# Optimization experiments

Hardware: AMD Instinct MI355X
Metric: run time of the kernel (lower is better)

The kernel has to match this reference:

```python
import jax, jax.numpy as jnp
import numpy as np

B, S, E, H = 1, 4096, 768, 12
D = E // H  # head_dim = 64


def setup_inputs() -> dict:
    key = jax.random.key(0)
    ks = jax.random.split(key, 6)
    scale = 0.02
    x = jax.random.normal(ks[0], (B, S, E), dtype=jnp.float32)
    Wq = jax.random.normal(ks[1], (E, E), dtype=jnp.float32) * scale
    Wk = jax.random.normal(ks[2], (E, E), dtype=jnp.float32) * scale
    Wv = jax.random.normal(ks[3], (E, E), dtype=jnp.float32) * scale
    Wo = jax.random.normal(ks[4], (E, E), dtype=jnp.float32) * scale
    bo = jax.random.normal(ks[5], (E,), dtype=jnp.float32) * scale
    mask = jnp.tril(jnp.ones((S, S), dtype=bool))[None, None]  # [1,1,S,S] causal
    return {"x": x, "Wq": Wq, "Wk": Wk, "Wv": Wv, "Wo": Wo, "bo": bo, "mask": mask}


def reference(x, Wq, Wk, Wv, Wo, bo, mask):
    # projections (torch Linear: y = x @ W.T; here W stored as [E,E] applied as x@W)
    q = jnp.einsum('bse,ef->bsf', x, Wq).reshape(B, S, H, D).transpose(0, 2, 1, 3)
    k = jnp.einsum('bse,ef->bsf', x, Wk).reshape(B, S, H, D).transpose(0, 2, 1, 3)
    v = jnp.einsum('bse,ef->bsf', x, Wv).reshape(B, S, H, D).transpose(0, 2, 1, 3)
    scores = jnp.einsum('bhqd,bhkd->bhqk', q, k) / jnp.sqrt(jnp.float32(D))
    scores = jnp.where(mask, scores, -jnp.inf)
    attn = jax.nn.softmax(scores, axis=-1)  # dropout p=0 -> identity
    ctx = jnp.einsum('bhqk,bhkd->bhqd', attn, v)
    ctx = ctx.transpose(0, 2, 1, 3).reshape(B, S, E)
    return jnp.einsum('bse,ef->bsf', ctx, Wo) + bo
```

## Files before the change

### kernel.cpp

```cpp
#include <hip/hip_runtime.h>
#include <math.h>

#define S 4096
#define E 768
#define H 12
#define Dh 64
#define SCALE2 0.1803368801111204f

typedef short short8 __attribute__((ext_vector_type(8)));
typedef float floatx4 __attribute__((ext_vector_type(4)));

__device__ __forceinline__ unsigned short f2bf(float f) {
    union { float f; unsigned int i; } c; c.f = f;
    unsigned int i = c.i;
    return (unsigned short)((i + 0x7fffu + ((i >> 16) & 1u)) >> 16);
}

__device__ __forceinline__ unsigned int pk_bf16(float lo, float hi) {
#if __has_builtin(__builtin_amdgcn_cvt_pk_bf16_f32)
    typedef __bf16 bf16x2 __attribute__((ext_vector_type(2)));
    union { bf16x2 v; unsigned int u; } c;
    c.v = __builtin_amdgcn_cvt_pk_bf16_f32(lo, hi);
    return c.u;
#else
    union { float f; unsigned int i; } a, b; a.f = lo; b.f = hi;
    return ((a.i + 0x8000u) >> 16) | ((b.i + 0x8000u) & 0xFFFF0000u);
#endif
}

__device__ __forceinline__ unsigned int scale_pk(unsigned int u, float s) {
    union { unsigned int i; float f; } lo, hi;
    lo.i = u << 16; hi.i = u & 0xffff0000u;
    return pk_bf16(lo.f * s, hi.f * s);
}

__device__ __forceinline__ void pk_atomic_add_bf16(unsigned short* addr, unsigned int bits) {
    unsigned long long a = (unsigned long long)addr;
    asm volatile("global_atomic_pk_add_bf16 %0, %1, off" :: "v"(a), "v"(bits) : "memory");
}

__device__ __forceinline__ void gload_lds16(const unsigned short* g, unsigned short* l) {
    __builtin_amdgcn_global_load_lds(
        (const __attribute__((address_space(1))) unsigned int*)g,
        (__attribute__((address_space(3))) unsigned int*)l, 16, 0, 0);
}

__device__ __forceinline__ void pl32swap(unsigned &a, unsigned &b) {
#if __has_builtin(__builtin_amdgcn_permlane32_swap)
    typedef unsigned uint2v __attribute__((ext_vector_type(2)));
    uint2v r = __builtin_amdgcn_permlane32_swap(a, b, false, false);
    a = r[0]; b = r[1];
#else
    asm("s_nop 1\n\tv_permlane32_swap_b32 %0, %1\n\ts_nop 1" : "+v"(a), "+v"(b));
#endif
}
__device__ __forceinline__ void pl16swap(unsigned &a, unsigned &b) {
#if __has_builtin(__builtin_amdgcn_permlane16_swap)
    typedef unsigned uint2v __attribute__((ext_vector_type(2)));
    uint2v r = __builtin_amdgcn_permlane16_swap(a, b, false, false);
    a = r[0]; b = r[1];
#else
    asm("s_nop 1\n\tv_permlane16_swap_b32 %0, %1\n\ts_nop 1" : "+v"(a), "+v"(b));
#endif
}

__device__ __forceinline__ short8 quad_redist(unsigned a0, unsigned a1, unsigned a2, unsigned a3) {
    pl32swap(a0, a2); pl16swap(a0, a2);
    pl32swap(a1, a3); pl16swap(a1, a3);
    union { unsigned u[4]; short8 s; } r;
    r.u[0] = a0; r.u[1] = a1; r.u[2] = a2; r.u[3] = a3;
    return r.s;
}

__global__ __launch_bounds__(256)
void prep_kernel(const float* __restrict__ x, unsigned short* __restrict__ xb,
                 const float* __restrict__ s0, const float* __restrict__ s1,
                 const float* __restrict__ s2, const float* __restrict__ s3,
                 unsigned short* __restrict__ d0, unsigned short* __restrict__ d1,
                 unsigned short* __restrict__ d2, unsigned short* __restrict__ d3,
                 char* __restrict__ zbase) {
    __shared__ unsigned short tile[32][33];
    const int b = blockIdx.x;
    const int tid = threadIdx.x;
    if (b < 2304) {
        int z = b / 576, rem = b - z * 576;
        int bx = rem % 24, by = rem / 24;
        const float* src = (z == 0) ? s0 : (z == 1) ? s1 : (z == 2) ? s2 : s3;
        unsigned short* dst = (z == 0) ? d0 : (z == 1) ? d1 : (z == 2) ? d2 : d3;
        int tx = tid & 31, ty = tid >> 5;
        int xcol = bx * 32 + tx;
        int y0 = by * 32;
        for (int j = ty; j < 32; j += 8)
            tile[j][tx] = f2bf(src[(size_t)(y0 + j) * E + xcol]);
        __syncthreads();
        int x2 = y0 + tx;
        int y2 = bx * 32;
        for (int j = ty; j < 32; j += 8)
            dst[(size_t)(y2 + j) * E + x2] = tile[tx][j];
    } else if (b < 3840) {
        int i = ((b - 2304) * 256 + tid) * 8;
        float4 f0 = *reinterpret_cast<const float4*>(x + i);
        float4 f1 = *reinterpret_cast<const float4*>(x + i + 4);
        unsigned short u[8];
        u[0]=f2bf(f0.x); u[1]=f2bf(f0.y); u[2]=f2bf(f0.z); u[3]=f2bf(f0.w);
        u[4]=f2bf(f1.x); u[5]=f2bf(f1.y); u[6]=f2bf(f1.z); u[7]=f2bf(f1.w);
        *reinterpret_cast<uint4*>(xb + i) = *reinterpret_cast<uint4*>(u);
    } else {
        size_t i = (size_t)(b - 3840) * 16384 + (size_t)tid * 64;
        uint4 z4 = make_uint4(0u, 0u, 0u, 0u);
        *reinterpret_cast<uint4*>(zbase + i)      = z4;
        *reinterpret_cast<uint4*>(zbase + i + 16) = z4;
        *reinterpret_cast<uint4*>(zbase + i + 32) = z4;
        *reinterpret_cast<uint4*>(zbase + i + 48) = z4;
    }
}

__global__ __launch_bounds__(256)
void gemm_qkv(const unsigned short* __restrict__ A,
              const unsigned short* __restrict__ BT,
              unsigned short* __restrict__ Qb, unsigned short* __restrict__ Kb,
              unsigned short* __restrict__ VTb) {
    __shared__ unsigned short Asm[2][128 * 64];
    __shared__ unsigned short Bsm[128 * 64];
    const int tid  = threadIdx.x;
    const int wave = tid >> 6, lane = tid & 63;
    const int quad = lane >> 4, l16 = lane & 15;
    const int lrow = lane >> 3, lchunk = lane & 7;
    const int bb = blockIdx.x;
    const int xcd = bb & 7, j = bb >> 3;
    const int mt = (xcd >> 1) * 8 + (j & 7);
    const int nt = (xcd & 1) * 9 + (j >> 3);
    const int n0 = nt * 128;
    const int m0 = mt * 128;
    const int aw = wave >> 1, bw = wave & 1;

    floatx4 acc[4][4];
    #pragma unroll
    for (int at = 0; at < 4; at++)
        #pragma unroll
        for (int ct = 0; ct < 4; ct++)
            #pragma unroll
            for (int r = 0; r < 4; r++) acc[at][ct][r] = 0.f;

    auto stageA = [&](int k0, int buf) {
        #pragma unroll
        for (int i = 0; i < 4; i++) {
            int rbase = wave * 32 + i * 8;
            int row   = rbase + lrow;
            int gc    = lchunk ^ (row & 7);
            gload_lds16(&A[(size_t)(m0 + row) * E + k0 + gc * 8], &Asm[buf][rbase * 64]);
        }
    };
    auto stageB = [&](int k0) {
        #pragma unroll
        for (int i = 0; i < 4; i++) {
            int rbase = wave * 32 + i * 8;
            int row   = rbase + lrow;
            int gc    = lchunk ^ (row & 7);
            gload_lds16(&BT[(size_t)(n0 + row) * E + k0 + gc * 8], &Bsm[rbase * 64]);
        }
    };

    stageA(0, 0);
    __builtin_amdgcn_sched_barrier(0);
    stageB(0);
    __builtin_amdgcn_sched_barrier(0);
    stageA(64, 1);
    __builtin_amdgcn_sched_barrier(0);

    for (int ki = 0; ki < 12; ki++) {
        const int cur = ki & 1;
        if (ki < 11) { asm volatile("s_waitcnt vmcnt(4)" ::: "memory"); }
        else         { asm volatile("s_waitcnt vmcnt(0)" ::: "memory"); }
        asm volatile("s_waitcnt lgkmcnt(0)" ::: "memory");
        __builtin_amdgcn_sched_barrier(0);
        __builtin_amdgcn_s_barrier();
        __builtin_amdgcn_sched_barrier(0);

        const unsigned short* As = Asm[cur];
        #pragma unroll
        for (int kk = 0; kk < 2; kk++) {
            const int g = kk * 4 + quad;
            short8 af[4], bfr[4];
            #pragma unroll
            for (int t = 0; t < 4; t++) {
                int ar = aw * 64 + t * 16 + l16;
                af[t]  = *reinterpret_cast<const short8*>(&As[ar * 64 + (g ^ (ar & 7)) * 8]);
                int br = bw * 64 + t * 16 + l16;
                bfr[t] = *reinterpret_cast<const short8*>(&Bsm[br * 64 + (g ^ (br & 7)) * 8]);
            }
            #pragma unroll
            for (int at = 0; at < 4; at++)
                #pragma unroll
                for (int ct = 0; ct < 4; ct++)
                    acc[at][ct] = __builtin_amdgcn_mfma_f32_16x16x32_bf16(af[at], bfr[ct], acc[at][ct], 0, 0, 0);
        }

        if (ki < 11) {
            __builtin_amdgcn_s_barrier();
            __builtin_amdgcn_sched_barrier(0);
            stageB((ki + 1) * 64);
            __builtin_amdgcn_sched_barrier(0);
            if (ki < 10) stageA((ki + 2) * 64, cur);
            __builtin_amdgcn_sched_barrier(0);
        }
    }

    const int sec = n0 / 768;
    const int nb  = n0 - sec * 768 + bw * 64;
    if (sec == 2) {
        #pragma unroll
        for (int at = 0; at < 4; at++)
            #pragma unroll
            for (int ct = 0; ct < 4; ct++) {
                int nsec = nb + ct * 16 + l16, hh = nsec >> 6, d = nsec & 63;
                int s0i = m0 + aw * 64 + at * 16 + quad * 4;
                uint2 w2;
                w2.x = pk_bf16(acc[at][ct][0], acc[at][ct][1]);
                w2.y = pk_bf16(acc[at][ct][2], acc[at][ct][3]);
                *reinterpret_cast<uint2*>(&VTb[(size_t)hh * Dh * S + (size_t)d * S + s0i]) = w2;
            }
    } else {
        #pragma unroll
        for (int at = 0; at < 4; at++)
            #pragma unroll
            for (int ct = 0; ct < 4; ct++) {
                int nsec = nb + ct * 16 + l16, hh = nsec >> 6, d = nsec & 63;
                #pragma unroll
                for (int r = 0; r < 4; r++) {
                    int s = m0 + aw * 64 + at * 16 + quad * 4 + r;
                    float v = acc[at][ct][r];
                    if (sec == 0) Qb[(size_t)hh * S * Dh + (size_t)s * Dh + d] = f2bf(v * SCALE2);
                    else          Kb[(size_t)hh * S * Dh + (size_t)s * Dh + d] = f2bf(v);
                }
            }
    }
}

__global__ __launch_bounds__(256)
void gemm_out(const unsigned short* __restrict__ ctxp,
              const unsigned short* __restrict__ BT,
              const float* __restrict__ lsumf,
              float* __restrict__ outp, const float* __restrict__ bias) {
    __shared__ unsigned short Asm[2][128 * 64];
    __shared__ unsigned short Bsm[2][64 * 64];
    const int tid  = threadIdx.x;
    const int wave = tid >> 6, lane = tid & 63;
    const int quad = lane >> 4, l16 = lane & 15;
    const int lrow = lane >> 3, lchunk = lane & 7;
    const int bb = blockIdx.x;
    const int xcd = bb & 7, j = bb >> 3;
    const int mt = (xcd >> 1) * 8 + (j & 7);
    const int nt = (xcd & 1) * 6 + (j >> 3);
    const int n0 = nt * 64;
    const int m0 = mt * 128;
    const int arow = tid >> 1, ahalf = tid & 1;

    floatx4 acc[2][4];
    #pragma unroll
    for (int at = 0; at < 2; at++)
        #pragma unroll
        for (int ct = 0; ct < 4; ct++)
            #pragma unroll
            for (int r = 0; r < 4; r++) acc[at][ct][r] = 0.f;

    uint4 au[4]; float lf;
    auto loadA = [&](int k0) {
        const unsigned short* asrc = ctxp + (size_t)(m0 + arow) * E + k0 + ahalf * 32;
        au[0] = *reinterpret_cast<const uint4*>(asrc + 0);
        au[1] = *reinterpret_cast<const uint4*>(asrc + 8);
        au[2] = *reinterpret_cast<const uint4*>(asrc + 16);
        au[3] = *reinterpret_cast<const uint4*>(asrc + 24);
        lf = lsumf[(k0 >> 6) * S + m0 + arow];
    };
    auto writeA = [&](int buf) {
        float linv = 1.0f / lf;
        #pragma unroll
        for (int cc = 0; cc < 4; cc++) {
            uint4 w;
            w.x = scale_pk(au[cc].x, linv);
            w.y = scale_pk(au[cc].y, linv);
            w.z = scale_pk(au[cc].z, linv);
            w.w = scale_pk(au[cc].w, linv);
            int chunk = ahalf * 4 + cc;
            *reinterpret_cast<uint4*>(&Asm[buf][arow * 64 + (chunk ^ (arow & 7)) * 8]) = w;
        }
    };
    auto stageB = [&](int k0, int buf) {
        #pragma unroll
        for (int i = 0; i < 2; i++) {
            int rbase = wave * 16 + i * 8;
            int row   = rbase + lrow;
            int gc    = lchunk ^ (row & 7);
            gload_lds16(&BT[(size_t)(n0 + row) * E + k0 + gc * 8], &Bsm[buf][rbase * 64]);
        }
    };

    loadA(0);
    __builtin_amdgcn_sched_barrier(0);
    asm volatile("s_waitcnt vmcnt(0)" ::: "memory");
    writeA(0);
    __builtin_amdgcn_sched_barrier(0);
    stageB(0, 0);
    __builtin_amdgcn_sched_barrier(0);
    loadA(64);
    __builtin_amdgcn_sched_barrier(0);

    for (int ki = 0; ki < 12; ki++) {
        const int cur = ki & 1, nxt = cur ^ 1;
        if (ki <= 10) { asm volatile("s_waitcnt vmcnt(5)" ::: "memory"); }
        else          { asm volatile("s_waitcnt vmcnt(0)" ::: "memory"); }
        asm volatile("s_waitcnt lgkmcnt(0)" ::: "memory");
        __builtin_amdgcn_sched_barrier(0);
        __builtin_amdgcn_s_barrier();
        __builtin_amdgcn_sched_barrier(0);
        asm volatile("s_waitcnt vmcnt(0)" ::: "memory");
        if (ki < 11) writeA(nxt);
        __builtin_amdgcn_sched_barrier(0);
        if (ki < 11) stageB((ki + 1) * 64, nxt);
        if (ki <= 9) loadA((ki + 2) * 64);
        __builtin_amdgcn_sched_barrier(0);

        const unsigned short* As = Asm[cur];
        const unsigned short* Bs = Bsm[cur];
        #pragma unroll
        for (int kk = 0; kk < 2; kk++) {
            const int g = kk * 4 + quad;
            short8 af[2], bfr[4];
            #pragma unroll
            for (int t = 0; t < 2; t++) {
                int ar = wave * 32 + t * 16 + l16;
                af[t] = *reinterpret_cast<const short8*>(&As[ar * 64 + (g ^ (ar & 7)) * 8]);
            }
            #pragma unroll
            for (int ct = 0; ct < 4; ct++) {
                int br = ct * 16 + l16;
                bfr[ct] = *reinterpret_cast<const short8*>(&Bs[br * 64 + (g ^ (br & 7)) * 8]);
            }
            #pragma unroll
            for (int at = 0; at < 2; at++)
                #pragma unroll
                for (int ct = 0; ct < 4; ct++)
                    acc[at][ct] = __builtin_amdgcn_mfma_f32_16x16x32_bf16(af[at], bfr[ct], acc[at][ct], 0, 0, 0);
        }
    }

    #pragma unroll
    for (int at = 0; at < 2; at++)
        #pragma unroll
        for (int ct = 0; ct < 4; ct++) {
            int n = n0 + ct * 16 + l16;
            float bn = bias[n];
            #pragma unroll
            for (int r = 0; r < 4; r++) {
                int s = m0 + wave * 32 + at * 16 + quad * 4 + r;
                outp[(size_t)s * E + n] = acc[at][ct][r] + bn;
            }
        }
}

__global__ __launch_bounds__(512, 4)
void attn_kernel(const unsigned short* __restrict__ Q,
                 const unsigned short* __restrict__ K,
                 const unsigned short* __restrict__ VT,
                 unsigned short* __restrict__ ctxp,
                 float* __restrict__ lsumf) {
    __shared__ unsigned short Ksm[3][128 * 64];
    __shared__ unsigned short Vsm[2][64 * 128];
    const int tid  = threadIdx.x;
    const int wave = tid >> 6, lane = tid & 63;
    const int quad = lane >> 4, l16 = lane & 15;
    const int lrow = lane >> 3, lchunk = lane & 7;

    const int b = blockIdx.x;
    const int w = b / H;
    const int h = b - w * H;
    int Qb, ck, nck;
    if      (w < 16) { Qb = 15 - (w >> 3);              ck = w & 7;  nck = 8; }
    else if (w < 30) { int u = w - 16; Qb = 13 - u / 7;   ck = u % 7; nck = 7; }
    else if (w < 42) { int u = w - 30; Qb = 11 - u / 6;   ck = u % 6; nck = 6; }
    else if (w < 52) { int u = w - 42; Qb = 9  - u / 5;   ck = u % 5; nck = 5; }
    else if (w < 60) { int u = w - 52; Qb = 7 - (u >> 2); ck = u & 3; nck = 4; }
    else if (w < 66) { int u = w - 60; Qb = 5 - u / 3;    ck = u % 3; nck = 3; }
    else if (w < 70) { int u = w - 66; Qb = 3 - (u >> 1); ck = u & 1; nck = 2; }
    else             { Qb = 1 - (w - 70);                 ck = 0;     nck = 1; }
    const int ntiles = 2 * Qb + 2;
    const int kt0 = (ntiles * ck) / nck;
    const int kt1 = (ntiles * (ck + 1)) / nck;

    const int qs = Qb * 256 + wave * 32;

    const unsigned short* Qh = Q  + (size_t)h * S * Dh;
    const unsigned short* Kh = K  + (size_t)h * S * Dh;
    const unsigned short* Vh = VT + (size_t)h * Dh * S;

    short8 bq[2][2];
    #pragma unroll
    for (int st = 0; st < 2; st++)
        #pragma unroll
        for (int c = 0; c < 2; c++)
            bq[st][c] = *reinterpret_cast<const short8*>(
                &Qh[(size_t)(qs + st * 16 + l16) * Dh + c * 32 + quad * 8]);

    float lsum[2] = {0.f, 0.f};
    floatx4 o[2][4];
    #pragma unroll
    for (int st = 0; st < 2; st++)
        #pragma unroll
        for (int ct = 0; ct < 4; ct++)
            #pragma unroll
            for (int r = 0; r < 4; r++) o[st][ct][r] = 0.f;

    auto stageK = [&](int kt, int buf) {
        #pragma unroll
        for (int i = 0; i < 2; i++) {
            int rbase = wave * 16 + i * 8;
            int row   = rbase + lrow;
            int gc    = lchunk ^ (row & 7);
            gload_lds16(&Kh[(size_t)(kt * 128 + row) * Dh + gc * 8], &Ksm[buf][rbase * 64]);
        }
    };
    auto stageV = [&](int kt, int buf) {
        #pragma unroll
        for (int i = 0; i < 2; i++) {
            int rbase = wave * 8 + i * 4;
            int row   = rbase + (lane >> 4);
            int c     = (lane & 15) ^ (row & 15);
            gload_lds16(&Vh[(size_t)row * S + kt * 128 + c * 8], &Vsm[buf][rbase * 128]);
        }
    };

    stageV(kt0, 0);
    stageK(kt0, 0);
    if (kt0 + 1 < kt1) stageK(kt0 + 1, 1);

    for (int kt = kt0; kt < kt1; kt++) {
        const int kc  = kt - kt0;
        const int kb3 = kc % 3;
        const int vb2 = kc & 1;
        if (kt + 1 < kt1) { asm volatile("s_waitcnt vmcnt(2)" ::: "memory"); }
        else              { asm volatile("s_waitcnt vmcnt(0)" ::: "memory"); }
        __builtin_amdgcn_sched_barrier(0);
        __builtin_amdgcn_s_barrier();
        __builtin_amdgcn_sched_barrier(0);
        if (kt + 1 < kt1) stageV(kt + 1, vb2 ^ 1);
        if (kt + 2 < kt1) stageK(kt + 2, (kb3 + 2) % 3);
        __builtin_amdgcn_sched_barrier(0);

        if (kt * 128 <= qs + 31) {
            #pragma unroll 1
            for (int hf = 0; hf < 2; hf++) {
                const int colbase = kt * 128 + hf * 64;
                if (colbase > qs + 31) break;

                floatx4 sc[2][4];
                #pragma unroll
                for (int st = 0; st < 2; st++)
                    #pragma unroll
                    for (int ct = 0; ct < 4; ct++)
                        #pragma unroll
                        for (int r = 0; r < 4; r++) sc[st][ct][r] = 0.f;
                __builtin_amdgcn_s_setprio(1);
                #pragma unroll
                for (int c = 0; c < 2; c++)
                    #pragma unroll
                    for (int ct = 0; ct < 4; ct++) {
                        int kr = hf * 64 + ct * 16 + l16;
                        short8 ak = *reinterpret_cast<const short8*>(
                            &Ksm[kb3][kr * 64 + (((c * 4 + quad) ^ (kr & 7))) * 8]);
                        sc[0][ct] = __builtin_amdgcn_mfma_f32_16x16x32_bf16(ak, bq[0][c], sc[0][ct], 0, 0, 0);
                        sc[1][ct] = __builtin_amdgcn_mfma_f32_16x16x32_bf16(ak, bq[1][c], sc[1][ct], 0, 0, 0);
                    }
                __builtin_amdgcn_s_setprio(0);

                if (colbase + 63 > qs) {
                    #pragma unroll
                    for (int st = 0; st < 2; st++) {
                        int qrow = qs + st * 16 + l16;
                        #pragma unroll
                        for (int ct = 0; ct < 4; ct++)
                            #pragma unroll
                            for (int r = 0; r < 4; r++) {
                                int kcol = colbase + ct * 16 + quad * 4 + r;
                                if (kcol > qrow) sc[st][ct][r] = -INFINITY;
                            }
                    }
                }

                unsigned Dp0[8], Dp1[8];
                #pragma unroll
                for (int ct = 0; ct < 4; ct++) {
                    float a0 = __builtin_amdgcn_exp2f(sc[0][ct][0]);
                    float a1 = __builtin_amdgcn_exp2f(sc[0][ct][1]);
                    float a2 = __builtin_amdgcn_exp2f(sc[0][ct][2]);
                    float a3 = __builtin_amdgcn_exp2f(sc[0][ct][3]);
                    lsum[0] += a0 + a1 + a2 + a3;
                    Dp0[ct * 2 + 0] = pk_bf16(a0, a1);
                    Dp0[ct * 2 + 1] = pk_bf16(a2, a3);
                    float b0 = __builtin_amdgcn_exp2f(sc[1][ct][0]);
                    float b1 = __builtin_amdgcn_exp2f(sc[1][ct][1]);
                    float b2 = __builtin_amdgcn_exp2f(sc[1][ct][2]);
                    float b3 = __builtin_amdgcn_exp2f(sc[1][ct][3]);
                    lsum[1] += b0 + b1 + b2 + b3;
                    Dp1[ct * 2 + 0] = pk_bf16(b0, b1);
                    Dp1[ct * 2 + 1] = pk_bf16(b2, b3);
                }

                __builtin_amdgcn_s_setprio(1);
                #pragma unroll
                for (int c = 0; c < 2; c++) {
                    short8 ap0 = quad_redist(Dp0[4*c+0], Dp0[4*c+1], Dp0[4*c+2], Dp0[4*c+3]);
                    short8 ap1 = quad_redist(Dp1[4*c+0], Dp1[4*c+1], Dp1[4*c+2], Dp1[4*c+3]);
                    #pragma unroll
                    for (int ct = 0; ct < 4; ct++) {
                        int vr = ct * 16 + l16;
                        short8 bv = *reinterpret_cast<const short8*>(
                            &Vsm[vb2][vr * 128 + (((hf * 8 + c * 4 + quad) ^ (vr & 15))) * 8]);
                        o[0][ct] = __builtin_amdgcn_mfma_f32_16x16x32_bf16(ap0, bv, o[0][ct], 0, 0, 0);
                        o[1][ct] = __builtin_amdgcn_mfma_f32_16x16x32_bf16(ap1, bv, o[1][ct], 0, 0, 0);
                    }
                }
                __builtin_amdgcn_s_setprio(0);
            }
        }
    }

    #pragma unroll
    for (int st = 0; st < 2; st++) {
        lsum[st] += __shfl_xor(lsum[st], 16, 64);
        lsum[st] += __shfl_xor(lsum[st], 32, 64);
    }
    if (quad == 0) {
        #pragma unroll
        for (int st = 0; st < 2; st++)
            atomicAdd(&lsumf[h * S + qs + st * 16 + l16], lsum[st]);
    }
    #pragma unroll
    for (int st = 0; st < 2; st++)
        #pragma unroll
        for (int r = 0; r < 4; r++) {
            int s = qs + st * 16 + quad * 4 + r;
            #pragma unroll
            for (int ct = 0; ct < 4; ct++) {
                float v  = o[st][ct][r];
                float vn = __shfl_xor(v, 1, 64);
                if ((l16 & 1) == 0)
                    pk_atomic_add_bf16(&ctxp[(size_t)s * E + h * Dh + ct * 16 + l16],
                                       pk_bf16(v, vn));
            }
        }
}

extern "C" void kernel_launch(void* const* d_in, const int* in_sizes, int n_in,
                              void* d_out, int out_size, void* d_ws, size_t ws_size,
                              hipStream_t stream) {
    const float* x  = (const float*)d_in[0];
    const float* Wq = (const float*)d_in[1];
    const float* Wk = (const float*)d_in[2];
    const float* Wv = (const float*)d_in[3];
    const float* Wo = (const float*)d_in[4];
    const float* bo = (const float*)d_in[5];
    float* out = (float*)d_out;

    char* ws = (char*)d_ws;
    const size_t WT = (size_t)E * E * 2;
    const size_t QB = (size_t)S * E * 2;
    unsigned short* WqT = (unsigned short*)(ws + 0 * WT);
    unsigned short* WkT = (unsigned short*)(ws + 1 * WT);
    unsigned short* WvT = (unsigned short*)(ws + 2 * WT);
    unsigned short* WoT = (unsigned short*)(ws + 3 * WT);
    unsigned short* xb  = (unsigned short*)(ws + 4 * WT + 0 * QB);
    unsigned short* Qbf = (unsigned short*)(ws + 4 * WT + 1 * QB);
    unsigned short* Kbf = (unsigned short*)(ws + 4 * WT + 2 * QB);
    unsigned short* VTb = (unsigned short*)(ws + 4 * WT + 3 * QB);
    unsigned short* ctxp  = (unsigned short*)(ws + 4 * WT + 4 * QB);
    float*          lsumf = (float*)(ws + 4 * WT + 5 * QB);

    prep_kernel<<<4236, 256, 0, stream>>>(
        x, xb, Wq, Wk, Wv, Wo, WqT, WkT, WvT, WoT, (char*)ctxp);

    gemm_qkv<<<576, 256, 0, stream>>>(xb, WqT, Qbf, Kbf, VTb);

    attn_kernel<<<864, 512, 0, stream>>>(Qbf, Kbf, VTb, ctxp, lsumf);

    gemm_out<<<384, 256, 0, stream>>>(ctxp, WoT, lsumf, out, bo);
}
```

Before: 221.5 us.

## Split attention waves across query and key halves for wider per-wave tiles

Each of the 8 waves now owns 64 query rows and one 64-column half of the 128-key tile, instead of 32 query rows over both halves. Every K fragment loaded from LDS therefore feeds four MFMAs instead of two, which cuts LDS read traffic per FLOP and removes the sequential inner loop over halves. The cost is doubled accumulator and score register state, which may raise register pressure under launch_bounds(512,4). Partial results from the two key halves are combined through the existing atomic adds on context and row sums, so the number of atomics per output row doubles.

After: 377.2 us. 70.3% more time.

```diff
diff --git a/kernel.cpp b/kernel.cpp
--- a/kernel.cpp
+++ b/kernel.cpp
@@ -371,6 +371,7 @@
     const int wave = tid >> 6, lane = tid & 63;
     const int quad = lane >> 4, l16 = lane & 15;
     const int lrow = lane >> 3, lchunk = lane & 7;
+    const int qw = wave >> 1, kw = wave & 1;
 
     const int b = blockIdx.x;
     const int w = b / H;
@@ -388,24 +389,24 @@
     const int kt0 = (ntiles * ck) / nck;
     const int kt1 = (ntiles * (ck + 1)) / nck;
 
-    const int qs = Qb * 256 + wave * 32;
+    const int qs = Qb * 256 + qw * 64;
 
     const unsigned short* Qh = Q  + (size_t)h * S * Dh;
     const unsigned short* Kh = K  + (size_t)h * S * Dh;
     const unsigned short* Vh = VT + (size_t)h * Dh * S;
 
-    short8 bq[2][2];
-    #pragma unroll
-    for (int st = 0; st < 2; st++)
+    short8 bq[4][2];
+    #pragma unroll
+    for (int st = 0; st < 4; st++)
         #pragma unroll
         for (int c = 0; c < 2; c++)
             bq[st][c] = *reinterpret_cast<const short8*>(
                 &Qh[(size_t)(qs + st * 16 + l16) * Dh + c * 32 + quad * 8]);
 
-    float lsum[2] = {0.f, 0.f};
-    floatx4 o[2][4];
-    #pragma unroll
-    for (int st = 0; st < 2; st++)
+    float lsum[4] = {0.f, 0.f, 0.f, 0.f};
+    floatx4 o[4][4];
+    #pragma unroll
+    for (int st = 0; st < 4; st++)
         #pragma unroll
         for (int ct = 0; ct < 4; ct++)
             #pragma unroll
@@ -447,96 +448,92 @@
         if (kt + 2 < kt1) stageK(kt + 2, (kb3 + 2) % 3);
         __builtin_amdgcn_sched_barrier(0);
 
-        if (kt * 128 <= qs + 31) {
-            #pragma unroll 1
-            for (int hf = 0; hf < 2; hf++) {
-                const int colbase = kt * 128 + hf * 64;
-                if (colbase > qs + 31) break;
-
-                floatx4 sc[2][4];
-                #pragma unroll
-                for (int st = 0; st < 2; st++)
+        const int colbase = kt * 128 + kw * 64;
+        if (colbase <= qs + 63) {
+            floatx4 sc[4][4];
+            #pragma unroll
+            for (int st = 0; st < 4; st++)
+                #pragma unroll
+                for (int ct = 0; ct < 4; ct++)
+                    #pragma unroll
+                    for (int r = 0; r < 4; r++) sc[st][ct][r] = 0.f;
+            __builtin_amdgcn_s_setprio(1);
+            #pragma unroll
+            for (int c = 0; c < 2; c++)
+                #pragma unroll
+                for (int ct = 0; ct < 4; ct++) {
+                    int kr = kw * 64 + ct * 16 + l16;
+                    short8 ak = *reinterpret_cast<const short8*>(
+                        &Ksm[kb3][kr * 64 + (((c * 4 + quad) ^ (kr & 7))) * 8]);
+                    sc[0][ct] = __builtin_amdgcn_mfma_f32_16x16x32_bf16(ak, bq[0][c], sc[0][ct], 0, 0, 0);
+                    sc[1][ct] = __builtin_amdgcn_mfma_f32_16x16x32_bf16(ak, bq[1][c], sc[1][ct], 0, 0, 0);
+                    sc[2][ct] = __builtin_amdgcn_mfma_f32_16x16x32_bf16(ak, bq[2][c], sc[2][ct], 0, 0, 0);
+                    sc[3][ct] = __builtin_amdgcn_mfma_f32_16x16x32_bf16(ak, bq[3][c], sc[3][ct], 0, 0, 0);
+                }
+            __builtin_amdgcn_s_setprio(0);
+
+            if (colbase + 63 > qs) {
+                #pragma unroll
+                for (int st = 0; st < 4; st++) {
+                    int qrow = qs + st * 16 + l16;
                     #pragma unroll
                     for (int ct = 0; ct < 4; ct++)
                         #pragma unroll
-                        for (int r = 0; r < 4; r++) sc[st][ct][r] = 0.f;
-                __builtin_amdgcn_s_setprio(1);
-                #pragma unroll
-                for (int c = 0; c < 2; c++)
-                    #pragma unroll
-                    for (int ct = 0; ct < 4; ct++) {
-                        int kr = hf * 64 + ct * 16 + l16;
-                        short8 ak = *reinterpret_cast<const short8*>(
-                            &Ksm[kb3][kr * 64 + (((c * 4 + quad) ^ (kr & 7))) * 8]);
-                        sc[0][ct] = __builtin_amdgcn_mfma_f32_16x16x32_bf16(ak, bq[0][c], sc[0][ct], 0, 0, 0);
-                        sc[1][ct] = __builtin_amdgcn_mfma_f32_16x16x32_bf16(ak, bq[1][c], sc[1][ct], 0, 0, 0);
-                    }
-                __builtin_amdgcn_s_setprio(0);
-
-                if (colbase + 63 > qs) {
-                    #pragma unroll
-                    for (int st = 0; st < 2; st++) {
-                        int qrow = qs + st * 16 + l16;
-                        #pragma unroll
-                        for (int ct = 0; ct < 4; ct++)
-                            #pragma unroll
-                            for (int r = 0; r < 4; r++) {
-                                int kcol = colbase + ct * 16 + quad * 4 + r;
-                                if (kcol > qrow) sc[st][ct][r] = -INFINITY;
-                            }
-                    }
+                        for (int r = 0; r < 4; r++) {
+                            int kcol = colbase + ct * 16 + quad * 4 + r;
+                            if (kcol > qrow) sc[st][ct][r] = -INFINITY;
+                        }
                 }
-
-                unsigned Dp0[8], Dp1[8];
+            }
+
+            unsigned Dp[4][8];
+            #pragma unroll
+            for (int st = 0; st < 4; st++)
                 #pragma unroll
                 for (int ct = 0; ct < 4; ct++) {
-                    float a0 = __builtin_amdgcn_exp2f(sc[0][ct][0]);
-                    float a1 = __builtin_amdgcn_exp2f(sc[0][ct][1]);
-                    float a2 = __builtin_amdgcn_exp2f(sc[0][ct][2]);
-                    float a3 = __builtin_amdgcn_exp2f(sc[0][ct][3]);
-                    lsum[0] += a0 + a1 + a2 + a3;
-                    Dp0[ct * 2 + 0] = pk_bf16(a0, a1);
-                    Dp0[ct * 2 + 1] = pk_bf16(a2, a3);
-                    float b0 = __builtin_amdgcn_exp2f(sc[1][ct][0]);
-                    float b1 = __builtin_amdgcn_exp2f(sc[1][ct][1]);
-                    float b2 = __builtin_amdgcn_exp2f(sc[1][ct][2]);
-                    float b3 = __builtin_amdgcn_exp2f(sc[1][ct][3]);
-                    lsum[1] += b0 + b1 + b2 + b3;
-                    Dp1[ct * 2 + 0] = pk_bf16(b0, b1);
-                    Dp1[ct * 2 + 1] = pk_bf16(b2, b3);
+                    float a0 = __builtin_amdgcn_exp2f(sc[st][ct][0]);
+                    float a1 = __builtin_amdgcn_exp2f(sc[st][ct][1]);
+                    float a2 = __builtin_amdgcn_exp2f(sc[st][ct][2]);
+                    float a3 = __builtin_amdgcn_exp2f(sc[st][ct][3]);
+                    lsum[st] += (a0 + a1) + (a2 + a3);
+                    Dp[st][ct * 2 + 0] = pk_bf16(a0, a1);
+                    Dp[st][ct * 2 + 1] = pk_bf16(a2, a3);
                 }
 
-                __builtin_amdgcn_s_setprio(1);
-                #pragma unroll
-                for (int c = 0; c < 2; c++) {
-                    short8 ap0 = quad_redist(Dp0[4*c+0], Dp0[4*c+1], Dp0[4*c+2], Dp0[4*c+3]);
-                    short8 ap1 = quad_redist(Dp1[4*c+0], Dp1[4*c+1], Dp1[4*c+2], Dp1[4*c+3]);
-                    #pragma unroll
-                    for (int ct = 0; ct < 4; ct++) {
-                        int vr = ct * 16 + l16;
-                        short8 bv = *reinterpret_cast<const short8*>(
-                            &Vsm[vb2][vr * 128 + (((hf * 8 + c * 4 + quad) ^ (vr & 15))) * 8]);
-                        o[0][ct] = __builtin_amdgcn_mfma_f32_16x16x32_bf16(ap0, bv, o[0][ct], 0, 0, 0);
-                        o[1][ct] = __builtin_amdgcn_mfma_f32_16x16x32_bf16(ap1, bv, o[1][ct], 0, 0, 0);
-                    }
+            __builtin_amdgcn_s_setprio(1);
+            #pragma unroll
+            for (int c = 0; c < 2; c++) {
+                short8 ap0 = quad_redist(Dp[0][4*c+0], Dp[0][4*c+1], Dp[0][4*c+2], Dp[0][4*c+3]);
+                short8 ap1 = quad_redist(Dp[1][4*c+0], Dp[1][4*c+1], Dp[1][4*c+2], Dp[1][4*c+3]);
+                short8 ap2 = quad_redist(Dp[2][4*c+0], Dp[2][4*c+1], Dp[2][4*c+2], Dp[2][4*c+3]);
+                short8 ap3 = quad_redist(Dp[3][4*c+0], Dp[3][4*c+1], Dp[3][4*c+2], Dp[3][4*c+3]);
+                #pragma unroll
+                for (int ct = 0; ct < 4; ct++) {
+                    int vr = ct * 16 + l16;
+                    short8 bv = *reinterpret_cast<const short8*>(
+                        &Vsm[vb2][vr * 128 + (((kw * 8 + c * 4 + quad) ^ (vr & 15))) * 8]);
+                    o[0][ct] = __builtin_amdgcn_mfma_f32_16x16x32_bf16(ap0, bv, o[0][ct], 0, 0, 0);
+                    o[1][ct] = __builtin_amdgcn_mfma_f32_16x16x32_bf16(ap1, bv, o[1][ct], 0, 0, 0);
+                    o[2][ct] = __builtin_amdgcn_mfma_f32_16x16x32_bf16(ap2, bv, o[2][ct], 0, 0, 0);
+                    o[3][ct] = __builtin_amdgcn_mfma_f32_16x16x32_bf16(ap3, bv, o[3][ct], 0, 0, 0);
                 }
-                __builtin_amdgcn_s_setprio(0);
-            }
-        }
-    }
-
-    #pragma unroll
-    for (int st = 0; st < 2; st++) {
+            }
+            __builtin_amdgcn_s_setprio(0);
+        }
+    }
+
+    #pragma unroll
+    for (int st = 0; st < 4; st++) {
         lsum[st] += __shfl_xor(lsum[st], 16, 64);
         lsum[st] += __shfl_xor(lsum[st], 32, 64);
     }
     if (quad == 0) {
         #pragma unroll
-        for (int st = 0; st < 2; st++)
+        for (int st = 0; st < 4; st++)
             atomicAdd(&lsumf[h * S + qs + st * 16 + l16], lsum[st]);
     }
     #pragma unroll
-    for (int st = 0; st < 2; st++)
+    for (int st = 0; st < 4; st++)
         #pragma unroll
         for (int r = 0; r < 4; r++) {
             int s = qs + st * 16 + quad * 4 + r;
```
